# Kernel optimization log

Hardware: AMD Instinct MI355X
Metric: run time of the kernel (lower is better)

The kernel has to match this reference:

```python
import jax, jax.numpy as jnp
import numpy as np

FEATURE_DIM = 256
LN_EPS = 1e-5        # torch nn.LayerNorm default
WHITEN_EPS = 1e-4    # whitening_eps init arg


def setup_inputs() -> dict:
    key = jax.random.key(0)
    k1, _ = jax.random.split(key)
    B, T, D = 64, 2048, FEATURE_DIM
    x = jax.random.normal(k1, (B, T, D), dtype=jnp.float32)
    gamma = jnp.ones((D,), dtype=jnp.float32)
    beta = jnp.zeros((D,), dtype=jnp.float32)
    return {"x": x, "gamma": gamma, "beta": beta}


def reference(x, gamma, beta):
    # x: (B, T, D)
    B, T, D = x.shape
    # LayerNorm over last dim
    mean = jnp.mean(x, axis=-1, keepdims=True)
    var = jnp.mean((x - mean) ** 2, axis=-1, keepdims=True)
    xn = (x - mean) * jax.lax.rsqrt(var + LN_EPS) * gamma + beta
    # Batched cross-frame covariance whitening (T >= 2 here)
    mu = jnp.mean(xn, axis=1, keepdims=True)          # (B, 1, D)
    xc = xn - mu                                       # (B, T, D)
    cov = jnp.einsum('btd,bte->bde', xc, xc) / (T - 1) # (B, D, D)
    cov = cov + WHITEN_EPS * jnp.eye(D, dtype=x.dtype)
    eigvals, eigvecs = jnp.linalg.eigh(cov)            # (B, D), (B, D, D)
    inv_sqrt_vals = jax.lax.rsqrt(jnp.clip(eigvals, WHITEN_EPS, None))  # (B, D)
    # inv_sqrt = V diag(w^-1/2) V^T
    inv_sqrt = jnp.einsum('bde,be,bfe->bdf', eigvecs, inv_sqrt_vals, eigvecs)
    out = jnp.einsum('btd,bdf->btf', xc, inv_sqrt)
    return out
```

## Files before the change

kernel.cpp:

```cpp
#include <hip/hip_runtime.h>
#include <cstddef>

#define TT 2048
#define BB 64
#define DD 256
#define LN_EPS 1e-5f
#define WEPS 1e-4f

typedef __attribute__((ext_vector_type(8))) short short8;
typedef __attribute__((ext_vector_type(4))) float f32x4;
typedef __attribute__((ext_vector_type(8))) _Float16 f16x8;
typedef __attribute__((ext_vector_type(4))) _Float16 f16x4;

__device__ __forceinline__ unsigned short f2h(float f) {
  _Float16 h = (_Float16)f;
  return *(unsigned short*)&h;
}
__device__ __forceinline__ float h2f(unsigned short u) {
  _Float16 h = *(_Float16*)&u;
  return (float)h;
}
__device__ __forceinline__ void gload16(unsigned short* lds, const unsigned short* g) {
  __builtin_amdgcn_global_load_lds(
      (const __attribute__((address_space(1))) void*)g,
      (__attribute__((address_space(3))) void*)lds, 16, 0, 0);
}

__global__ __launch_bounds__(256) void prepass_kernel(const float* __restrict__ x,
    float* __restrict__ stats, float* __restrict__ part) {
  int c = blockIdx.x;
  int b = blockIdx.y;
  int tid = threadIdx.x;
  int wave = tid >> 6, lane = tid & 63;
  int rowbase = b * TT + c * 128 + wave * 32;
  const float* xb = x + (size_t)rowbase * DD + lane * 4;
  float a0 = 0.f, a1 = 0.f, a2 = 0.f, a3 = 0.f;
  for (int i = 0; i < 32; ++i) {
    float4 v = *(const float4*)&xb[(size_t)i * DD];
    float s  = v.x + v.y + v.z + v.w;
    float sq = v.x*v.x + v.y*v.y + v.z*v.z + v.w*v.w;
    #pragma unroll
    for (int off = 32; off; off >>= 1) { s += __shfl_xor(s, off); sq += __shfl_xor(sq, off); }
    float mean = s * (1.f/DD);
    float var  = fmaxf(sq * (1.f/DD) - mean*mean, 0.f);
    float rstd = rsqrtf(var + LN_EPS);
    if (lane == 0) {
      stats[2*(rowbase+i)]   = mean;
      stats[2*(rowbase+i)+1] = rstd;
    }
    a0 += (v.x - mean) * rstd;
    a1 += (v.y - mean) * rstd;
    a2 += (v.z - mean) * rstd;
    a3 += (v.w - mean) * rstd;
  }
  int pidx = c * 4 + wave;
  *(float4*)&part[((size_t)pidx*BB + b)*DD + lane*4] = make_float4(a0, a1, a2, a3);
}

__global__ __launch_bounds__(256) void mu_finalize_kernel(const float* __restrict__ part,
                                                          const float* __restrict__ gamma,
                                                          const float* __restrict__ beta,
                                                          float* __restrict__ mu) {
  int b = blockIdx.x;
  int d = threadIdx.x;
  float s = 0.f;
  #pragma unroll 8
  for (int c = 0; c < 64; ++c) s += part[((size_t)c*BB + b)*DD + d];
  mu[b*DD + d] = gamma[d] * s * (1.f/TT) + beta[d];
}

__global__ __launch_bounds__(256) void cov_mfma(const float* __restrict__ x,
    const float* __restrict__ stats, const float* __restrict__ gamma,
    const float* __restrict__ beta, const float* __restrict__ mu,
    unsigned short* __restrict__ Ch) {
  int flat = blockIdx.y * gridDim.x + blockIdx.x;
  int kx = flat & 7, j = flat >> 3;
  int b = (kx << 3) + j / 10;
  int tile = j - (j / 10) * 10;
  int p = 0, t = tile;
  while (t >= 4 - p) { t -= (4 - p); ++p; }
  int q = p + t;
  int i0 = p * 64, j0 = q * 64;
  bool diag = (p == q);

  __shared__ unsigned short sm[8448];
  unsigned short* sA = sm;
  unsigned short* sB = sm + 4096;
  __shared__ float sGi[64], sBi[64], sGj[64], sBj[64];

  int tid = threadIdx.x;
  const float* mub = mu + (size_t)b*DD;
  if (tid < 64) {
    sGi[tid] = gamma[i0+tid]; sBi[tid] = beta[i0+tid] - mub[i0+tid];
    sGj[tid] = gamma[j0+tid]; sBj[tid] = beta[j0+tid] - mub[j0+tid];
  }
  __syncthreads();

  int wave = tid >> 6, lane = tid & 63;
  int lr = lane & 15, lg = lane >> 4;
  int tg4 = tid >> 4;
  int dg  = tid & 15;
  int d0 = dg * 4;
  const float* xb  = x + (size_t)b*TT*DD;
  const float* stb = stats + (size_t)b*TT*2;

  float4 gi4 = *(const float4*)&sGi[d0];
  float4 bi4 = *(const float4*)&sBi[d0];
  float4 gj4 = *(const float4*)&sGj[d0];
  float4 bj4 = *(const float4*)&sBj[d0];

  int ch16 = tg4 >> 1, half = tg4 & 1;
  int widx[4];
  #pragma unroll
  for (int jj = 0; jj < 4; ++jj) {
    int dl = d0 + jj;
    int swz = (ch16 ^ (dl & 7) ^ ((dl >> 3) & 7)) & 7;
    widx[jj] = dl*64 + swz*8 + half*4;
  }

  f32x4 acc[4] = {};

  for (int k0 = 0; k0 < TT; k0 += 64) {
    int trow = k0 + tg4 * 4;
    float4 s01 = *(const float4*)&stb[2*trow];
    float4 s23 = *(const float4*)&stb[2*trow + 4];
    float mm[4] = {s01.x, s01.z, s23.x, s23.z};
    float rr[4] = {s01.y, s01.w, s23.y, s23.w};
    {
      _Float16 va[4][4];
      #pragma unroll
      for (int i = 0; i < 4; ++i) {
        float4 v = *(const float4*)&xb[(size_t)(trow+i)*DD + i0 + d0];
        va[i][0] = (_Float16)(((v.x - mm[i]) * rr[i]) * gi4.x + bi4.x);
        va[i][1] = (_Float16)(((v.y - mm[i]) * rr[i]) * gi4.y + bi4.y);
        va[i][2] = (_Float16)(((v.z - mm[i]) * rr[i]) * gi4.z + bi4.z);
        va[i][3] = (_Float16)(((v.w - mm[i]) * rr[i]) * gi4.w + bi4.w);
      }
      #pragma unroll
      for (int jj = 0; jj < 4; ++jj) {
        f16x4 w = {va[0][jj], va[1][jj], va[2][jj], va[3][jj]};
        *(f16x4*)&sA[widx[jj]] = w;
      }
    }
    if (!diag) {
      _Float16 vb[4][4];
      #pragma unroll
      for (int i = 0; i < 4; ++i) {
        float4 v = *(const float4*)&xb[(size_t)(trow+i)*DD + j0 + d0];
        vb[i][0] = (_Float16)(((v.x - mm[i]) * rr[i]) * gj4.x + bj4.x);
        vb[i][1] = (_Float16)(((v.y - mm[i]) * rr[i]) * gj4.y + bj4.y);
        vb[i][2] = (_Float16)(((v.z - mm[i]) * rr[i]) * gj4.z + bj4.z);
        vb[i][3] = (_Float16)(((v.w - mm[i]) * rr[i]) * gj4.w + bj4.w);
      }
      #pragma unroll
      for (int jj = 0; jj < 4; ++jj) {
        f16x4 w = {vb[0][jj], vb[1][jj], vb[2][jj], vb[3][jj]};
        *(f16x4*)&sB[widx[jj]] = w;
      }
    }
    __syncthreads();
    const unsigned short* pB = diag ? sA : sB;
    #pragma unroll
    for (int ks = 0; ks < 2; ++ks) {
      int rowA = wave*16 + lr;
      int cc = ks*4 + lg;
      int aoff = rowA*64 + (((cc ^ (rowA&7) ^ ((rowA>>3)&7)) & 7) << 3);
      f16x8 av = *(const f16x8*)&sA[aoff];
      #pragma unroll
      for (int n = 0; n < 4; ++n) {
        int rowB = n*16 + lr;
        int boff = rowB*64 + (((cc ^ (rowB&7) ^ ((rowB>>3)&7)) & 7) << 3);
        f16x8 bv = *(const f16x8*)&pB[boff];
        acc[n] = __builtin_amdgcn_mfma_f32_16x16x32_f16(av, bv, acc[n], 0, 0, 0);
      }
    }
    __syncthreads();
  }

  float* sC = (float*)sm;
  #pragma unroll
  for (int n = 0; n < 4; ++n)
    #pragma unroll
    for (int r = 0; r < 4; ++r)
      sC[(wave*16 + lg*4 + r)*65 + n*16 + lr] = acc[n][r];
  __syncthreads();
  unsigned short* Chb = Ch + (size_t)b*DD*DD;
  const float invTm1 = 1.f / (float)(TT - 1);
  int row = tid >> 2, cb = (tid & 3) * 16;
  int gi = i0 + row;
  unsigned short hv[16];
  #pragma unroll
  for (int e = 0; e < 16; ++e) {
    float v = sC[row*65 + cb + e] * invTm1;
    int gj = j0 + cb + e;
    if (gi == gj) v += WEPS;
    hv[e] = f2h(v);
    if (!diag) Chb[(size_t)gj*DD + gi] = hv[e];
  }
  size_t go = (size_t)gi*DD + j0 + cb;
  *(short8*)&Chb[go]     = *(short8*)&hv[0];
  *(short8*)&Chb[go + 8] = *(short8*)&hv[8];
}

__global__ __launch_bounds__(256) void power_kernel(
    const unsigned short* __restrict__ Ch, float* __restrict__ sbuf) {
  int b = blockIdx.x, tid = threadIdx.x;
  __shared__ unsigned short sC[DD*DD];
  __shared__ float v[DD];
  __shared__ float red[4];
  const unsigned short* Cb = Ch + (size_t)b*DD*DD;
  #pragma unroll
  for (int i = 0; i < 32; ++i) {
    int chunkid = i*256 + tid;
    int r = chunkid >> 5, ch = chunkid & 31;
    short8 qv = *(const short8*)&Cb[(size_t)chunkid*8];
    *(short8*)&sC[r*256 + ((ch ^ (r & 7)) << 3)] = qv;
  }
  unsigned u = (unsigned)tid * 2654435761u;
  v[tid] = 0.5f + (float)((u >> 9) & 1023) * (1.f/1024.f);
  __syncthreads();
  float lam = 1.f;
  for (int it = 0; it < 10; ++it) {
    float w = 0.f;
    #pragma unroll
    for (int ch = 0; ch < 32; ++ch) {
      short8 hq = *(const short8*)&sC[tid*256 + ((ch ^ (tid & 7)) << 3)];
      const float* vp = &v[ch*8];
      #pragma unroll
      for (int e = 0; e < 8; ++e) w += h2f((unsigned short)hq[e]) * vp[e];
    }
    float ssq = w * w;
    #pragma unroll
    for (int off = 32; off; off >>= 1) ssq += __shfl_xor(ssq, off);
    if ((tid & 63) == 0) red[tid >> 6] = ssq;
    __syncthreads();
    float nrm = sqrtf(red[0] + red[1] + red[2] + red[3]);
    lam = nrm;
    v[tid] = w / nrm;
    __syncthreads();
  }
  if (tid == 0) sbuf[b] = lam * 1.12f;
}

__global__ __launch_bounds__(256) void ew1_kernel(const unsigned short* __restrict__ C,
    unsigned short* __restrict__ M1, unsigned short* __restrict__ Z1,
    const float* __restrict__ sbuf) {
  int b = blockIdx.y;
  int chunk = blockIdx.x * 256 + threadIdx.x;
  int row = chunk >> 5, cb = (chunk & 31) * 8;
  float inv = 1.f / sbuf[b];
  size_t off = (size_t)b*DD*DD + (size_t)chunk*8;
  short8 cv = *(const short8*)&C[off];
  unsigned short mo[8], zo[8];
  #pragma unroll
  for (int e = 0; e < 8; ++e) {
    float c = h2f((unsigned short)cv[e]) * inv;
    float dg = (row == cb + e) ? 1.f : 0.f;
    mo[e] = f2h(3.f*dg - c);
    zo[e] = f2h(1.5f*dg - 0.5f*c);
  }
  *(short8*)&M1[off] = *(short8*)&mo[0];
  *(short8*)&Z1[off] = *(short8*)&zo[0];
}

__device__ __forceinline__ void bgemm_tile2(
    const unsigned short* __restrict__ A, const unsigned short* __restrict__ B,
    unsigned short* __restrict__ C,
    float alpha, float diagBeta, int tilex, int b, unsigned short* sm) {
  unsigned short* sA = sm;
  unsigned short* sB = sm + 8192;

  const int tid = threadIdx.x;
  const int i0g = (tilex >> 1) * 128, j0g = (tilex & 1) * 128;
  const size_t mb = (size_t)b * DD * DD;
  const int wave = tid >> 6, lane = tid & 63;
  const int wr = wave >> 2, wc = wave & 3;
  const int lr = lane & 15, lg = lane >> 4;

  f32x4 acc[8] = {};

  for (int k0 = 0; k0 < DD; k0 += 64) {
    #pragma unroll
    for (int p2 = 0; p2 < 2; ++p2) {
      int slot = tid + p2 * 512;
      int row = slot >> 3, c = slot & 7;
      int srcc = (c ^ (row & 7)) << 3;
      size_t ga = mb + (size_t)(i0g + row) * DD + k0 + srcc;
      size_t gb = mb + (size_t)(j0g + row) * DD + k0 + srcc;
      int base = (wave * 64 + p2 * 512) * 8;
      gload16(&sA[base], A + ga);
      gload16(&sB[base], B + gb);
    }
    __syncthreads();
    #pragma unroll
    for (int ks = 0; ks < 2; ++ks) {
      int cc = ks * 4 + lg;
      f16x8 bv[2];
      #pragma unroll
      for (int n = 0; n < 2; ++n) {
        int rowB = wc * 32 + n * 16 + lr;
        int boff = rowB * 64 + ((cc ^ (rowB & 7)) * 8);
        bv[n] = *(const f16x8*)&sB[boff];
      }
      #pragma unroll
      for (int m = 0; m < 4; ++m) {
        int rowA = wr * 64 + m * 16 + lr;
        int aoff = rowA * 64 + ((cc ^ (rowA & 7)) * 8);
        f16x8 av = *(const f16x8*)&sA[aoff];
        #pragma unroll
        for (int n = 0; n < 2; ++n)
          acc[m*2+n] = __builtin_amdgcn_mfma_f32_16x16x32_f16(av, bv[n], acc[m*2+n], 0, 0, 0);
      }
    }
    __syncthreads();
  }

  #pragma unroll
  for (int m = 0; m < 4; ++m) {
    #pragma unroll
    for (int n = 0; n < 2; ++n) {
      int col = j0g + wc * 32 + n * 16 + lr;
      int row0 = i0g + wr * 64 + m * 16 + lg * 4;
      #pragma unroll
      for (int r = 0; r < 4; ++r) {
        float vv = alpha * acc[m*2+n][r];
        int row = row0 + r;
        if (row == col) vv += diagBeta;
        C[mb + (size_t)row * DD + col] = f2h(vv);
      }
    }
  }
}

__global__ __launch_bounds__(512) void bgemm_mfma2(
    const unsigned short* __restrict__ A, const unsigned short* __restrict__ B,
    unsigned short* __restrict__ C, float alpha, float diagBeta) {
  __shared__ unsigned short sm[16384];
  int flat = blockIdx.y * gridDim.x + blockIdx.x;
  int kx = flat & 7, j = flat >> 3;
  int b = (kx << 3) + (j >> 2);
  int tile = j & 3;
  bgemm_tile2(A, B, C, alpha, diagBeta, tile, b, sm);
}

__global__ __launch_bounds__(512) void bgemm_y1(
    const unsigned short* __restrict__ A, const unsigned short* __restrict__ B,
    unsigned short* __restrict__ C, const float* __restrict__ sbuf) {
  __shared__ unsigned short sm[16384];
  int flat = blockIdx.y * gridDim.x + blockIdx.x;
  int kx = flat & 7, j = flat >> 3;
  int b = (kx << 3) + (j >> 2);
  int tile = j & 3;
  float alpha = 0.5f / sbuf[b];
  bgemm_tile2(A, B, C, alpha, 0.f, tile, b, sm);
}

__global__ __launch_bounds__(512) void bgemm_dual2(
    const unsigned short* __restrict__ A0, const unsigned short* __restrict__ B0,
    unsigned short* __restrict__ C0,
    const unsigned short* __restrict__ A1, const unsigned short* __restrict__ B1,
    unsigned short* __restrict__ C1) {
  __shared__ unsigned short sm[16384];
  int flat = blockIdx.y * gridDim.x + blockIdx.x;
  int kx = flat & 7, j = flat >> 3;
  int b = (kx << 3) + (j >> 3);
  int t8 = j & 7;
  int half = t8 >> 2, tile = t8 & 3;
  if (half == 0)
    bgemm_tile2(A0, B0, C0, 0.5f, 0.f, tile, b, sm);
  else
    bgemm_tile2(A1, B1, C1, 0.5f, 0.f, tile, b, sm);
}

__global__ __launch_bounds__(512) void out_mfma2(const float* __restrict__ x,
    const float* __restrict__ stats, const float* __restrict__ gamma,
    const float* __restrict__ beta, const float* __restrict__ mu,
    const unsigned short* __restrict__ Z, const float* __restrict__ sbuf,
    float* __restrict__ out) {
  int flat = blockIdx.y * gridDim.x + blockIdx.x;
  int kx = flat & 7, j = flat >> 3;
  int b = (kx << 3) + (j >> 5);
  int tile = j & 31;
  int t0 = (tile >> 1) * 128, f0 = (tile & 1) * 128;
  __shared__ unsigned short sm[16384];
  unsigned short* sA = sm;
  unsigned short* sB = sm + 8192;
  __shared__ float sG[256], sBs[256];

  int tid = threadIdx.x;
  if (tid < 256) {
    sG[tid] = gamma[tid];
    sBs[tid] = beta[tid] - mu[(size_t)b*DD + tid];
  } else {
    int d = tid - 256;
    (void)d;
  }
  if (tid >= 256) {
  }
  __syncthreads();

  const int wave = tid >> 6, lane = tid & 63;
  const int wr = wave >> 2, wc = wave & 3;
  const int lr = lane & 15, lg = lane >> 4;
  const float* xb  = x + (size_t)b*TT*DD;
  const float* stb = stats + (size_t)b*TT*2;
  const unsigned short* Zb = Z + (size_t)b*DD*DD;

  f32x4 acc[8] = {};

  for (int k0 = 0; k0 < DD; k0 += 64) {
    #pragma unroll
    for (int p2 = 0; p2 < 2; ++p2) {
      int slot = tid + p2 * 512;
      int row = slot >> 3, c0 = slot & 7;
      int srcc = (c0 ^ (row & 7)) << 3;
      size_t gz = (size_t)(f0 + row) * DD + k0 + srcc;
      int base = (wave * 64 + p2 * 512) * 8;
      gload16(&sB[base], Zb + gz);
      int trow = t0 + row;
      float mean = stb[2*trow], rstd = stb[2*trow+1];
      const float* xr = xb + (size_t)trow*DD + k0 + c0*8;
      _Float16 h8[8];
      #pragma unroll
      for (int qq = 0; qq < 2; ++qq) {
        float4 v = *(const float4*)&xr[qq*4];
        float vv[4] = {v.x, v.y, v.z, v.w};
        #pragma unroll
        for (int e2 = 0; e2 < 4; ++e2) {
          int d = k0 + c0*8 + qq*4 + e2;
          h8[qq*4+e2] = (_Float16)((vv[e2] - mean) * rstd * sG[d] + sBs[d]);
        }
      }
      int ld = row * 64 + ((c0 ^ (row & 7)) * 8);
      *(f16x8*)&sA[ld] = *(f16x8*)&h8[0];
    }
    __syncthreads();
    #pragma unroll
    for (int ks = 0; ks < 2; ++ks) {
      int cc = ks * 4 + lg;
      f16x8 bv[2];
      #pragma unroll
      for (int n = 0; n < 2; ++n) {
        int rowB = wc * 32 + n * 16 + lr;
        int boff = rowB * 64 + ((cc ^ (rowB & 7)) * 8);
        bv[n] = *(const f16x8*)&sB[boff];
      }
      #pragma unroll
      for (int m = 0; m < 4; ++m) {
        int rowA = wr * 64 + m * 16 + lr;
        int aoff = rowA * 64 + ((cc ^ (rowA & 7)) * 8);
        f16x8 av = *(const f16x8*)&sA[aoff];
        #pragma unroll
        for (int n = 0; n < 2; ++n)
          acc[m*2+n] = __builtin_amdgcn_mfma_f32_16x16x32_f16(av, bv[n], acc[m*2+n], 0, 0, 0);
      }
    }
    __syncthreads();
  }

  float rs = rsqrtf(sbuf[b]);
  float* ob = out + (size_t)b*TT*DD;
  #pragma unroll
  for (int m = 0; m < 4; ++m) {
    #pragma unroll
    for (int n = 0; n < 2; ++n) {
      int col = f0 + wc * 32 + n * 16 + lr;
      int row0 = t0 + wr * 64 + m * 16 + lg * 4;
      #pragma unroll
      for (int r = 0; r < 4; ++r)
        ob[(size_t)(row0 + r)*DD + col] = acc[m*2+n][r] * rs;
    }
  }
}

extern "C" void kernel_launch(void* const* d_in, const int* in_sizes, int n_in,
                              void* d_out, int out_size, void* d_ws, size_t ws_size,
                              hipStream_t stream) {
  const float* x     = (const float*)d_in[0];
  const float* gamma = (const float*)d_in[1];
  const float* beta  = (const float*)d_in[2];
  float* out = (float*)d_out;

  float* wsf   = (float*)d_ws;
  float* stats = wsf;
  float* mu    = wsf + 262144;
  float* sbuf  = wsf + 278528;
  unsigned short* nsb = (unsigned short*)(wsf + 278784);
  const size_t MATU = (size_t)BB * DD * DD;
  unsigned short* H[5];
  for (int k = 0; k < 5; ++k) H[k] = nsb + (size_t)k * MATU;
  float* part = (float*)H[1];

  prepass_kernel<<<dim3(16, BB), 256, 0, stream>>>(x, stats, part);
  mu_finalize_kernel<<<BB, 256, 0, stream>>>(part, gamma, beta, mu);
  cov_mfma<<<dim3(10, BB), 256, 0, stream>>>(x, stats, gamma, beta, mu, H[0]);
  power_kernel<<<BB, 256, 0, stream>>>(H[0], sbuf);

  ew1_kernel<<<dim3(32, BB), 256, 0, stream>>>(H[0], H[2], H[1], sbuf);
  bgemm_y1<<<dim3(4, BB), 512, 0, stream>>>(H[0], H[2], H[3], sbuf);

  bgemm_mfma2<<<dim3(4, BB), 512, 0, stream>>>(H[1], H[3], H[2], -1.f, 3.f);
  bgemm_dual2<<<dim3(8, BB), 512, 0, stream>>>(H[3], H[2], H[0], H[2], H[1], H[4]);
  bgemm_mfma2<<<dim3(4, BB), 512, 0, stream>>>(H[4], H[0], H[2], -1.f, 3.f);
  bgemm_dual2<<<dim3(8, BB), 512, 0, stream>>>(H[0], H[2], H[3], H[2], H[4], H[1]);
  bgemm_mfma2<<<dim3(4, BB), 512, 0, stream>>>(H[1], H[3], H[2], -1.f, 3.f);
  bgemm_dual2<<<dim3(8, BB), 512, 0, stream>>>(H[3], H[2], H[0], H[2], H[1], H[4]);
  bgemm_mfma2<<<dim3(4, BB), 512, 0, stream>>>(H[4], H[0], H[2], -1.f, 3.f);
  bgemm_mfma2<<<dim3(4, BB), 512, 0, stream>>>(H[2], H[4], H[1], 0.5f, 0.f);

  out_mfma2<<<dim3(32, BB), 512, 0, stream>>>(x, stats, gamma, beta, mu, H[1], sbuf, out);
}
```

Baseline: 237.3 us.

## Fuse power iteration and Newton-Schulz chain into one cooperative kernel

Replaces the power-iteration kernel, the elementwise init kernel and the ten batched GEMM launches with a single cooperative kernel of 256 blocks that uses grid-wide syncs between stages. The aim is to remove repeated launch overhead and inter-kernel gaps on the serial chain of small 256x256 matrix products. In exchange, the dual GEMM stages now run two tiles sequentially per block instead of spreading them across 512 blocks. Shared memory per block also grows to 128 KB, which limits occupancy to one block per CU, and each grid.sync adds a barrier cost.

```diff
diff --git a/kernel.cpp b/kernel.cpp
--- a/kernel.cpp
+++ b/kernel.cpp
@@ -1,4 +1,5 @@
 #include <hip/hip_runtime.h>
+#include <hip/hip_cooperative_groups.h>
 #include <cstddef>
 
 #define TT 2048
@@ -6,6 +7,8 @@
 #define DD 256
 #define LN_EPS 1e-5f
 #define WEPS 1e-4f
+
+namespace cg = cooperative_groups;
 
 typedef __attribute__((ext_vector_type(8))) short short8;
 typedef __attribute__((ext_vector_type(4))) float f32x4;
@@ -202,67 +205,6 @@
   *(short8*)&Chb[go + 8] = *(short8*)&hv[8];
 }
 
-__global__ __launch_bounds__(256) void power_kernel(
-    const unsigned short* __restrict__ Ch, float* __restrict__ sbuf) {
-  int b = blockIdx.x, tid = threadIdx.x;
-  __shared__ unsigned short sC[DD*DD];
-  __shared__ float v[DD];
-  __shared__ float red[4];
-  const unsigned short* Cb = Ch + (size_t)b*DD*DD;
-  #pragma unroll
-  for (int i = 0; i < 32; ++i) {
-    int chunkid = i*256 + tid;
-    int r = chunkid >> 5, ch = chunkid & 31;
-    short8 qv = *(const short8*)&Cb[(size_t)chunkid*8];
-    *(short8*)&sC[r*256 + ((ch ^ (r & 7)) << 3)] = qv;
-  }
-  unsigned u = (unsigned)tid * 2654435761u;
-  v[tid] = 0.5f + (float)((u >> 9) & 1023) * (1.f/1024.f);
-  __syncthreads();
-  float lam = 1.f;
-  for (int it = 0; it < 10; ++it) {
-    float w = 0.f;
-    #pragma unroll
-    for (int ch = 0; ch < 32; ++ch) {
-      short8 hq = *(const short8*)&sC[tid*256 + ((ch ^ (tid & 7)) << 3)];
-      const float* vp = &v[ch*8];
-      #pragma unroll
-      for (int e = 0; e < 8; ++e) w += h2f((unsigned short)hq[e]) * vp[e];
-    }
-    float ssq = w * w;
-    #pragma unroll
-    for (int off = 32; off; off >>= 1) ssq += __shfl_xor(ssq, off);
-    if ((tid & 63) == 0) red[tid >> 6] = ssq;
-    __syncthreads();
-    float nrm = sqrtf(red[0] + red[1] + red[2] + red[3]);
-    lam = nrm;
-    v[tid] = w / nrm;
-    __syncthreads();
-  }
-  if (tid == 0) sbuf[b] = lam * 1.12f;
-}
-
-__global__ __launch_bounds__(256) void ew1_kernel(const unsigned short* __restrict__ C,
-    unsigned short* __restrict__ M1, unsigned short* __restrict__ Z1,
-    const float* __restrict__ sbuf) {
-  int b = blockIdx.y;
-  int chunk = blockIdx.x * 256 + threadIdx.x;
-  int row = chunk >> 5, cb = (chunk & 31) * 8;
-  float inv = 1.f / sbuf[b];
-  size_t off = (size_t)b*DD*DD + (size_t)chunk*8;
-  short8 cv = *(const short8*)&C[off];
-  unsigned short mo[8], zo[8];
-  #pragma unroll
-  for (int e = 0; e < 8; ++e) {
-    float c = h2f((unsigned short)cv[e]) * inv;
-    float dg = (row == cb + e) ? 1.f : 0.f;
-    mo[e] = f2h(3.f*dg - c);
-    zo[e] = f2h(1.5f*dg - 0.5f*c);
-  }
-  *(short8*)&M1[off] = *(short8*)&mo[0];
-  *(short8*)&Z1[off] = *(short8*)&zo[0];
-}
-
 __device__ __forceinline__ void bgemm_tile2(
     const unsigned short* __restrict__ A, const unsigned short* __restrict__ B,
     unsigned short* __restrict__ C,
@@ -332,44 +274,104 @@
   }
 }
 
-__global__ __launch_bounds__(512) void bgemm_mfma2(
-    const unsigned short* __restrict__ A, const unsigned short* __restrict__ B,
-    unsigned short* __restrict__ C, float alpha, float diagBeta) {
-  __shared__ unsigned short sm[16384];
-  int flat = blockIdx.y * gridDim.x + blockIdx.x;
-  int kx = flat & 7, j = flat >> 3;
-  int b = (kx << 3) + (j >> 2);
-  int tile = j & 3;
-  bgemm_tile2(A, B, C, alpha, diagBeta, tile, b, sm);
-}
-
-__global__ __launch_bounds__(512) void bgemm_y1(
-    const unsigned short* __restrict__ A, const unsigned short* __restrict__ B,
-    unsigned short* __restrict__ C, const float* __restrict__ sbuf) {
-  __shared__ unsigned short sm[16384];
-  int flat = blockIdx.y * gridDim.x + blockIdx.x;
-  int kx = flat & 7, j = flat >> 3;
-  int b = (kx << 3) + (j >> 2);
-  int tile = j & 3;
-  float alpha = 0.5f / sbuf[b];
-  bgemm_tile2(A, B, C, alpha, 0.f, tile, b, sm);
-}
-
-__global__ __launch_bounds__(512) void bgemm_dual2(
-    const unsigned short* __restrict__ A0, const unsigned short* __restrict__ B0,
-    unsigned short* __restrict__ C0,
-    const unsigned short* __restrict__ A1, const unsigned short* __restrict__ B1,
-    unsigned short* __restrict__ C1) {
-  __shared__ unsigned short sm[16384];
-  int flat = blockIdx.y * gridDim.x + blockIdx.x;
-  int kx = flat & 7, j = flat >> 3;
-  int b = (kx << 3) + (j >> 3);
-  int t8 = j & 7;
-  int half = t8 >> 2, tile = t8 & 3;
-  if (half == 0)
-    bgemm_tile2(A0, B0, C0, 0.5f, 0.f, tile, b, sm);
-  else
-    bgemm_tile2(A1, B1, C1, 0.5f, 0.f, tile, b, sm);
+__global__ void __launch_bounds__(512, 1) ns_chain(
+    unsigned short* H0, unsigned short* H1, unsigned short* H2,
+    unsigned short* H3, unsigned short* H4, float* sbuf) {
+  cg::grid_group grid = cg::this_grid();
+  __shared__ unsigned short sm[65536];
+  __shared__ float vv[DD];
+  __shared__ float red[4];
+  const int blk = blockIdx.x;
+  const int tid = threadIdx.x;
+
+  if (blk < BB) {
+    const unsigned short* Cb = H0 + (size_t)blk*DD*DD;
+    #pragma unroll
+    for (int i = 0; i < 16; ++i) {
+      int chunkid = i*512 + tid;
+      int r = chunkid >> 5, ch = chunkid & 31;
+      short8 qv = *(const short8*)&Cb[(size_t)chunkid*8];
+      *(short8*)&sm[r*256 + ((ch ^ (r & 7)) << 3)] = qv;
+    }
+    if (tid < DD) {
+      unsigned u = (unsigned)tid * 2654435761u;
+      vv[tid] = 0.5f + (float)((u >> 9) & 1023) * (1.f/1024.f);
+    }
+    __syncthreads();
+    float lam = 1.f;
+    for (int it = 0; it < 10; ++it) {
+      float w = 0.f;
+      if (tid < DD) {
+        #pragma unroll
+        for (int ch = 0; ch < 32; ++ch) {
+          short8 hq = *(const short8*)&sm[tid*256 + ((ch ^ (tid & 7)) << 3)];
+          const float* vp = &vv[ch*8];
+          #pragma unroll
+          for (int e = 0; e < 8; ++e) w += h2f((unsigned short)hq[e]) * vp[e];
+        }
+      }
+      float ssq = w * w;
+      #pragma unroll
+      for (int off = 32; off; off >>= 1) ssq += __shfl_xor(ssq, off);
+      if (tid < DD && (tid & 63) == 0) red[tid >> 6] = ssq;
+      __syncthreads();
+      float nrm = sqrtf(red[0] + red[1] + red[2] + red[3]);
+      lam = nrm;
+      if (tid < DD) vv[tid] = w / nrm;
+      __syncthreads();
+    }
+    if (tid == 0) sbuf[blk] = lam * 1.12f;
+  }
+  grid.sync();
+
+  {
+    #pragma unroll
+    for (int i = 0; i < 4; ++i) {
+      int chunk = blk*2048 + i*512 + tid;
+      int b = chunk >> 13;
+      int within = chunk & 8191;
+      int row = within >> 5, cb = (within & 31) * 8;
+      float inv = 1.f / sbuf[b];
+      size_t off = (size_t)chunk * 8;
+      short8 cv = *(const short8*)&H0[off];
+      unsigned short mo[8], zo[8];
+      #pragma unroll
+      for (int e = 0; e < 8; ++e) {
+        float c = h2f((unsigned short)cv[e]) * inv;
+        float dg = (row == cb + e) ? 1.f : 0.f;
+        mo[e] = f2h(3.f*dg - c);
+        zo[e] = f2h(1.5f*dg - 0.5f*c);
+      }
+      *(short8*)&H2[off] = *(short8*)&mo[0];
+      *(short8*)&H1[off] = *(short8*)&zo[0];
+    }
+  }
+  grid.sync();
+
+  int kx = blk & 7, j = blk >> 3;
+  int gb = (kx << 3) + (j >> 2);
+  int gtile = j & 3;
+
+  bgemm_tile2(H0, H2, H3, 0.5f / sbuf[gb], 0.f, gtile, gb, sm);
+  grid.sync();
+  bgemm_tile2(H1, H3, H2, -1.f, 3.f, gtile, gb, sm);
+  grid.sync();
+  bgemm_tile2(H3, H2, H0, 0.5f, 0.f, gtile, gb, sm);
+  bgemm_tile2(H2, H1, H4, 0.5f, 0.f, gtile, gb, sm);
+  grid.sync();
+  bgemm_tile2(H4, H0, H2, -1.f, 3.f, gtile, gb, sm);
+  grid.sync();
+  bgemm_tile2(H0, H2, H3, 0.5f, 0.f, gtile, gb, sm);
+  bgemm_tile2(H2, H4, H1, 0.5f, 0.f, gtile, gb, sm);
+  grid.sync();
+  bgemm_tile2(H1, H3, H2, -1.f, 3.f, gtile, gb, sm);
+  grid.sync();
+  bgemm_tile2(H3, H2, H0, 0.5f, 0.f, gtile, gb, sm);
+  bgemm_tile2(H2, H1, H4, 0.5f, 0.f, gtile, gb, sm);
+  grid.sync();
+  bgemm_tile2(H4, H0, H2, -1.f, 3.f, gtile, gb, sm);
+  grid.sync();
+  bgemm_tile2(H2, H4, H1, 0.5f, 0.f, gtile, gb, sm);
 }
 
 __global__ __launch_bounds__(512) void out_mfma2(const float* __restrict__ x,
@@ -391,11 +393,6 @@
   if (tid < 256) {
     sG[tid] = gamma[tid];
     sBs[tid] = beta[tid] - mu[(size_t)b*DD + tid];
-  } else {
-    int d = tid - 256;
-    (void)d;
-  }
-  if (tid >= 256) {
   }
   __syncthreads();
 
@@ -424,11 +421,11 @@
       #pragma unroll
       for (int qq = 0; qq < 2; ++qq) {
         float4 v = *(const float4*)&xr[qq*4];
-        float vv[4] = {v.x, v.y, v.z, v.w};
+        float vvv[4] = {v.x, v.y, v.z, v.w};
         #pragma unroll
         for (int e2 = 0; e2 < 4; ++e2) {
           int d = k0 + c0*8 + qq*4 + e2;
-          h8[qq*4+e2] = (_Float16)((vv[e2] - mean) * rstd * sG[d] + sBs[d]);
+          h8[qq*4+e2] = (_Float16)((vvv[e2] - mean) * rstd * sG[d] + sBs[d]);
         }
       }
       int ld = row * 64 + ((c0 ^ (row & 7)) * 8);
@@ -494,19 +491,11 @@
   prepass_kernel<<<dim3(16, BB), 256, 0, stream>>>(x, stats, part);
   mu_finalize_kernel<<<BB, 256, 0, stream>>>(part, gamma, beta, mu);
   cov_mfma<<<dim3(10, BB), 256, 0, stream>>>(x, stats, gamma, beta, mu, H[0]);
-  power_kernel<<<BB, 256, 0, stream>>>(H[0], sbuf);
-
-  ew1_kernel<<<dim3(32, BB), 256, 0, stream>>>(H[0], H[2], H[1], sbuf);
-  bgemm_y1<<<dim3(4, BB), 512, 0, stream>>>(H[0], H[2], H[3], sbuf);
-
-  bgemm_mfma2<<<dim3(4, BB), 512, 0, stream>>>(H[1], H[3], H[2], -1.f, 3.f);
-  bgemm_dual2<<<dim3(8, BB), 512, 0, stream>>>(H[3], H[2], H[0], H[2], H[1], H[4]);
-  bgemm_mfma2<<<dim3(4, BB), 512, 0, stream>>>(H[4], H[0], H[2], -1.f, 3.f);
-  bgemm_dual2<<<dim3(8, BB), 512, 0, stream>>>(H[0], H[2], H[3], H[2], H[4], H[1]);
-  bgemm_mfma2<<<dim3(4, BB), 512, 0, stream>>>(H[1], H[3], H[2], -1.f, 3.f);
-  bgemm_dual2<<<dim3(8, BB), 512, 0, stream>>>(H[3], H[2], H[0], H[2], H[1], H[4]);
-  bgemm_mfma2<<<dim3(4, BB), 512, 0, stream>>>(H[4], H[0], H[2], -1.f, 3.f);
-  bgemm_mfma2<<<dim3(4, BB), 512, 0, stream>>>(H[2], H[4], H[1], 0.5f, 0.f);
+
+  unsigned short *h0 = H[0], *h1 = H[1], *h2 = H[2], *h3 = H[3], *h4 = H[4];
+  float* sb = sbuf;
+  void* kargs[] = {&h0, &h1, &h2, &h3, &h4, &sb};
+  hipLaunchCooperativeKernel((void*)ns_chain, dim3(256), dim3(512), kargs, 0, stream);
 
   out_mfma2<<<dim3(32, BB), 512, 0, stream>>>(x, stats, gamma, beta, mu, H[1], sbuf, out);
 }
```

Result: slower. 632.9 us (+166.7%).

## Fuse first Newton-Schulz step into C·C GEMM, tighten scaling, drop one iteration

Applied to the files above, without the earlier changes.

The separate elementwise kernel and first GEMM of the Newton-Schulz inverse-sqrt iteration become a single kernel. It computes C·C and forms Y1 and Z1 algebraically in the epilogue, so M1 is never materialised. The spectral-bound safety factor drops from 1.12 to 1.05, which lets the loop drop one dual-GEMM and one GEMM launch. Fewer iterations reduce launches and matrix traffic but risk lower accuracy if convergence is not complete.

```diff
diff --git a/kernel.cpp b/kernel.cpp
--- a/kernel.cpp
+++ b/kernel.cpp
@@ -239,28 +239,7 @@
     v[tid] = w / nrm;
     __syncthreads();
   }
-  if (tid == 0) sbuf[b] = lam * 1.12f;
-}
-
-__global__ __launch_bounds__(256) void ew1_kernel(const unsigned short* __restrict__ C,
-    unsigned short* __restrict__ M1, unsigned short* __restrict__ Z1,
-    const float* __restrict__ sbuf) {
-  int b = blockIdx.y;
-  int chunk = blockIdx.x * 256 + threadIdx.x;
-  int row = chunk >> 5, cb = (chunk & 31) * 8;
-  float inv = 1.f / sbuf[b];
-  size_t off = (size_t)b*DD*DD + (size_t)chunk*8;
-  short8 cv = *(const short8*)&C[off];
-  unsigned short mo[8], zo[8];
-  #pragma unroll
-  for (int e = 0; e < 8; ++e) {
-    float c = h2f((unsigned short)cv[e]) * inv;
-    float dg = (row == cb + e) ? 1.f : 0.f;
-    mo[e] = f2h(3.f*dg - c);
-    zo[e] = f2h(1.5f*dg - 0.5f*c);
-  }
-  *(short8*)&M1[off] = *(short8*)&mo[0];
-  *(short8*)&Z1[off] = *(short8*)&zo[0];
+  if (tid == 0) sbuf[b] = lam * 1.05f;
 }
 
 __device__ __forceinline__ void bgemm_tile2(
@@ -341,18 +320,6 @@
   int b = (kx << 3) + (j >> 2);
   int tile = j & 3;
   bgemm_tile2(A, B, C, alpha, diagBeta, tile, b, sm);
-}
-
-__global__ __launch_bounds__(512) void bgemm_y1(
-    const unsigned short* __restrict__ A, const unsigned short* __restrict__ B,
-    unsigned short* __restrict__ C, const float* __restrict__ sbuf) {
-  __shared__ unsigned short sm[16384];
-  int flat = blockIdx.y * gridDim.x + blockIdx.x;
-  int kx = flat & 7, j = flat >> 3;
-  int b = (kx << 3) + (j >> 2);
-  int tile = j & 3;
-  float alpha = 0.5f / sbuf[b];
-  bgemm_tile2(A, B, C, alpha, 0.f, tile, b, sm);
 }
 
 __global__ __launch_bounds__(512) void bgemm_dual2(
@@ -372,6 +339,85 @@
     bgemm_tile2(A1, B1, C1, 0.5f, 0.f, tile, b, sm);
 }
 
+__global__ __launch_bounds__(512) void bgemm_p0(
+    const unsigned short* __restrict__ C, unsigned short* __restrict__ Y1,
+    unsigned short* __restrict__ Z1, const float* __restrict__ sbuf) {
+  __shared__ unsigned short sm[16384];
+  unsigned short* sA = sm;
+  unsigned short* sB = sm + 8192;
+  int flat = blockIdx.y * gridDim.x + blockIdx.x;
+  int kx = flat & 7, j = flat >> 3;
+  int b = (kx << 3) + (j >> 2);
+  int tilex = j & 3;
+
+  const int tid = threadIdx.x;
+  const int i0g = (tilex >> 1) * 128, j0g = (tilex & 1) * 128;
+  const size_t mb = (size_t)b * DD * DD;
+  const int wave = tid >> 6, lane = tid & 63;
+  const int wr = wave >> 2, wc = wave & 3;
+  const int lr = lane & 15, lg = lane >> 4;
+
+  f32x4 acc[8] = {};
+
+  for (int k0 = 0; k0 < DD; k0 += 64) {
+    #pragma unroll
+    for (int p2 = 0; p2 < 2; ++p2) {
+      int slot = tid + p2 * 512;
+      int row = slot >> 3, c = slot & 7;
+      int srcc = (c ^ (row & 7)) << 3;
+      size_t ga = mb + (size_t)(i0g + row) * DD + k0 + srcc;
+      size_t gb = mb + (size_t)(j0g + row) * DD + k0 + srcc;
+      int base = (wave * 64 + p2 * 512) * 8;
+      gload16(&sA[base], C + ga);
+      gload16(&sB[base], C + gb);
+    }
+    __syncthreads();
+    #pragma unroll
+    for (int ks = 0; ks < 2; ++ks) {
+      int cc = ks * 4 + lg;
+      f16x8 bv[2];
+      #pragma unroll
+      for (int n = 0; n < 2; ++n) {
+        int rowB = wc * 32 + n * 16 + lr;
+        int boff = rowB * 64 + ((cc ^ (rowB & 7)) * 8);
+        bv[n] = *(const f16x8*)&sB[boff];
+      }
+      #pragma unroll
+      for (int m = 0; m < 4; ++m) {
+        int rowA = wr * 64 + m * 16 + lr;
+        int aoff = rowA * 64 + ((cc ^ (rowA & 7)) * 8);
+        f16x8 av = *(const f16x8*)&sA[aoff];
+        #pragma unroll
+        for (int n = 0; n < 2; ++n)
+          acc[m*2+n] = __builtin_amdgcn_mfma_f32_16x16x32_f16(av, bv[n], acc[m*2+n], 0, 0, 0);
+      }
+    }
+    __syncthreads();
+  }
+
+  float invs = 1.f / sbuf[b];
+  float a2 = -0.5f * invs * invs;
+  float a1c = 1.5f * invs;
+  float z1c = -0.5f * invs;
+  #pragma unroll
+  for (int m = 0; m < 4; ++m) {
+    #pragma unroll
+    for (int n = 0; n < 2; ++n) {
+      int col = j0g + wc * 32 + n * 16 + lr;
+      int row0 = i0g + wr * 64 + m * 16 + lg * 4;
+      #pragma unroll
+      for (int r = 0; r < 4; ++r) {
+        int row = row0 + r;
+        float cv = h2f(C[mb + (size_t)row * DD + col]);
+        float yv = a2 * acc[m*2+n][r] + a1c * cv;
+        float zv = z1c * cv + ((row == col) ? 1.5f : 0.f);
+        Y1[mb + (size_t)row * DD + col] = f2h(yv);
+        Z1[mb + (size_t)row * DD + col] = f2h(zv);
+      }
+    }
+  }
+}
+
 __global__ __launch_bounds__(512) void out_mfma2(const float* __restrict__ x,
     const float* __restrict__ stats, const float* __restrict__ gamma,
     const float* __restrict__ beta, const float* __restrict__ mu,
@@ -391,11 +437,6 @@
   if (tid < 256) {
     sG[tid] = gamma[tid];
     sBs[tid] = beta[tid] - mu[(size_t)b*DD + tid];
-  } else {
-    int d = tid - 256;
-    (void)d;
-  }
-  if (tid >= 256) {
   }
   __syncthreads();
 
@@ -424,11 +465,11 @@
       #pragma unroll
       for (int qq = 0; qq < 2; ++qq) {
         float4 v = *(const float4*)&xr[qq*4];
-        float vv[4] = {v.x, v.y, v.z, v.w};
+        float vvv[4] = {v.x, v.y, v.z, v.w};
         #pragma unroll
         for (int e2 = 0; e2 < 4; ++e2) {
           int d = k0 + c0*8 + qq*4 + e2;
-          h8[qq*4+e2] = (_Float16)((vv[e2] - mean) * rstd * sG[d] + sBs[d]);
+          h8[qq*4+e2] = (_Float16)((vvv[e2] - mean) * rstd * sG[d] + sBs[d]);
         }
       }
       int ld = row * 64 + ((c0 ^ (row & 7)) * 8);
@@ -496,17 +537,13 @@
   cov_mfma<<<dim3(10, BB), 256, 0, stream>>>(x, stats, gamma, beta, mu, H[0]);
   power_kernel<<<BB, 256, 0, stream>>>(H[0], sbuf);
 
-  ew1_kernel<<<dim3(32, BB), 256, 0, stream>>>(H[0], H[2], H[1], sbuf);
-  bgemm_y1<<<dim3(4, BB), 512, 0, stream>>>(H[0], H[2], H[3], sbuf);
-
+  bgemm_p0<<<dim3(4, BB), 512, 0, stream>>>(H[0], H[3], H[1], sbuf);
   bgemm_mfma2<<<dim3(4, BB), 512, 0, stream>>>(H[1], H[3], H[2], -1.f, 3.f);
   bgemm_dual2<<<dim3(8, BB), 512, 0, stream>>>(H[3], H[2], H[0], H[2], H[1], H[4]);
   bgemm_mfma2<<<dim3(4, BB), 512, 0, stream>>>(H[4], H[0], H[2], -1.f, 3.f);
   bgemm_dual2<<<dim3(8, BB), 512, 0, stream>>>(H[0], H[2], H[3], H[2], H[4], H[1]);
   bgemm_mfma2<<<dim3(4, BB), 512, 0, stream>>>(H[1], H[3], H[2], -1.f, 3.f);
-  bgemm_dual2<<<dim3(8, BB), 512, 0, stream>>>(H[3], H[2], H[0], H[2], H[1], H[4]);
-  bgemm_mfma2<<<dim3(4, BB), 512, 0, stream>>>(H[4], H[0], H[2], -1.f, 3.f);
-  bgemm_mfma2<<<dim3(4, BB), 512, 0, stream>>>(H[2], H[4], H[1], 0.5f, 0.f);
-
-  out_mfma2<<<dim3(32, BB), 512, 0, stream>>>(x, stats, gamma, beta, mu, H[1], sbuf, out);
-}
+  bgemm_mfma2<<<dim3(4, BB), 512, 0, stream>>>(H[2], H[1], H[4], 0.5f, 0.f);
+
+  out_mfma2<<<dim3(32, BB), 512, 0, stream>>>(x, stats, gamma, beta, mu, H[4], sbuf, out);
+}
```

New measurement: 218.5 us. 1.09x faster.
